# Optimization experiments

Hardware: AMD Instinct MI355X
Metric: run time of the kernel (lower is better)

Reference implementation:

```python
import jax, jax.numpy as jnp
import numpy as np

N, FIN, H, FOUT = 4096, 128, 4, 64
NEG_INF = -1e9


def _xavier(key, shape):
    fan_in, fan_out = shape[-2], shape[-1]
    limit = float(np.sqrt(6.0 / (fan_in + fan_out)))
    return jax.random.uniform(key, shape, jnp.float32, -limit, limit)


def setup_inputs() -> dict:
    key = jax.random.key(0)
    ks = jax.random.split(key, 7)
    x = jax.random.normal(ks[0], (N, FIN), jnp.float32)
    u = jax.random.uniform(ks[1], (N, N))
    mask = jnp.where(u < 0.02, 0.0, NEG_INF).astype(jnp.float32)
    idx = jnp.arange(N)
    mask = mask.at[idx, idx].set(0.0)
    proj_param = _xavier(ks[2], (H, FIN, FOUT))          # per-head projection
    score_src = _xavier(ks[3], (H, FOUT, 1))             # scoring_fn_source (IMP1 layout)
    score_tgt = _xavier(ks[4], (H, FOUT, 1))             # scoring_fn_target
    skip_w = _xavier(ks[5], (H * FOUT, FIN))             # skip_proj Linear weight
    bias = jnp.zeros((H * FOUT,), jnp.float32)
    return {"x": x, "mask": mask, "proj_param": proj_param,
            "score_src": score_src, "score_tgt": score_tgt,
            "skip_w": skip_w, "bias": bias}


def reference(x, mask, proj_param, score_src, score_tgt, skip_w, bias):
    # project: [1,N,Fin] @ [H,Fin,Fout] -> [H,N,Fout]
    h = jnp.einsum('nf,hfo->hno', x, proj_param)
    # additive (Bahdanau-style) scores
    s_src = jnp.matmul(h, score_src)                     # [H,N,1]
    s_tgt = jnp.matmul(h, score_tgt)                     # [H,N,1]
    all_scores = jax.nn.leaky_relu(s_src + jnp.swapaxes(s_tgt, 1, 2), 0.2)  # [H,N,N]
    attn = jax.nn.softmax(all_scores + mask[None, :, :], axis=-1)           # [H,N,N]
    # aggregate: [H,N,N] @ [H,N,Fout] -> [N,H,Fout]
    out = jnp.einsum('hnm,hmo->nho', attn, h)
    # skip connection (dims differ: Fin != H*Fout -> use skip_proj)
    out = out + jnp.matmul(x, skip_w.T).reshape(N, H, FOUT)
    out = out.reshape(N, H * FOUT) + bias                # concat heads + bias
    return jax.nn.elu(out)
```

## Files before the change

kernel.cpp:

```cpp
#include <hip/hip_runtime.h>
#include <hip/hip_bf16.h>
#include <math.h>


#define NN   4096
#define FIN  128
#define NH   4
#define FO   64
#define HF   256
#define MAXNBR 384

__global__ __launch_bounds__(256) void k1_gemm(
        const float* __restrict__ x,
        const float* __restrict__ proj,
        const float* __restrict__ skw,
        float* __restrict__ h_ws, float* __restrict__ skip_ws) {
    __shared__ float sA[64 * 132];
    __shared__ float sB[128 * 64];
    const int tid = threadIdx.x;
    const int bc  = blockIdx.x;
    const int i0  = blockIdx.y * 64;

    {
        const float4* src = (const float4*)(x + (size_t)i0 * FIN);
        #pragma unroll
        for (int q = 0; q < 8; q++) {
            int s   = tid + q * 256;
            int row = s >> 5;
            int c4  = (s & 31) << 2;
            float4 v = src[s];
            float* d = sA + row * 132 + c4;
            d[0] = v.x; d[1] = v.y; d[2] = v.z; d[3] = v.w;
        }
    }
    if (bc < 4) {
        const float4* src = (const float4*)(proj + (size_t)bc * FIN * FO);
        #pragma unroll
        for (int q = 0; q < 8; q++) {
            int s = tid + q * 256;
            *(float4*)(sB + (size_t)s * 4) = src[s];
        }
    } else {
        const float* sw = skw + (size_t)(bc - 4) * 64 * FIN;
        #pragma unroll
        for (int q = 0; q < 8; q++) {
            int s  = tid + q * 256;
            int c  = s & 63;
            int k4 = (s >> 6) << 2;
            float4 v = *(const float4*)(sw + (size_t)c * FIN + k4);
            sB[(k4 + 0) * 64 + c] = v.x;
            sB[(k4 + 1) * 64 + c] = v.y;
            sB[(k4 + 2) * 64 + c] = v.z;
            sB[(k4 + 3) * 64 + c] = v.w;
        }
    }
    __syncthreads();

    const int tx = tid & 15, ty = tid >> 4;
    const int r0 = ty << 2, c0 = tx << 2;
    float acc[4][4] = {};
    #pragma unroll 2
    for (int k = 0; k < FIN; k += 4) {
        alignas(16) float a[4][4];
        alignas(16) float b[4][4];
        #pragma unroll
        for (int rr = 0; rr < 4; rr++)
            *(float4*)a[rr] = *(const float4*)(sA + (r0 + rr) * 132 + k);
        #pragma unroll
        for (int kk = 0; kk < 4; kk++)
            *(float4*)b[kk] = *(const float4*)(sB + (k + kk) * 64 + c0);
        #pragma unroll
        for (int kk = 0; kk < 4; kk++)
            #pragma unroll
            for (int rr = 0; rr < 4; rr++)
                #pragma unroll
                for (int cc = 0; cc < 4; cc++)
                    acc[rr][cc] = fmaf(a[rr][kk], b[kk][cc], acc[rr][cc]);
    }

    if (bc < 4) {
        float* dst = h_ws + (size_t)bc * (NN * FO) + (size_t)i0 * FO;
        #pragma unroll
        for (int rr = 0; rr < 4; rr++)
            *(float4*)(dst + (size_t)(r0 + rr) * FO + c0) = *(float4*)acc[rr];
    } else {
        float* dst = skip_ws + (size_t)i0 * HF + (bc - 4) * 64;
        #pragma unroll
        for (int rr = 0; rr < 4; rr++)
            *(float4*)(dst + (size_t)(r0 + rr) * HF + c0) = *(float4*)acc[rr];
    }
}

__global__ __launch_bounds__(256) void k1b_scores(
        const float* __restrict__ h_ws,
        const float* __restrict__ asrc, const float* __restrict__ atgt,
        float* __restrict__ src4, float* __restrict__ tgt4) {
    const int lane = threadIdx.x & 63;
    const int w    = threadIdx.x >> 6;
    const int i    = blockIdx.x * 4 + w;
    float ss[4], tt[4];
    #pragma unroll
    for (int hh = 0; hh < 4; hh++) {
        float hv = h_ws[(size_t)hh * (NN * FO) + (size_t)i * FO + lane];
        float sv = hv * asrc[hh * FO + lane];
        float tv = hv * atgt[hh * FO + lane];
        #pragma unroll
        for (int off = 32; off >= 1; off >>= 1) {
            sv += __shfl_xor(sv, off, 64);
            tv += __shfl_xor(tv, off, 64);
        }
        ss[hh] = sv; tt[hh] = tv;
    }
    if (lane == 0) {
        *(float4*)(src4 + (size_t)i * 4) = make_float4(ss[0], ss[1], ss[2], ss[3]);
        *(float4*)(tgt4 + (size_t)i * 4) = make_float4(tt[0], tt[1], tt[2], tt[3]);
    }
}

__global__ __launch_bounds__(256) void k2_attn(
        const unsigned int* __restrict__ mask,
        const float* __restrict__ h_ws,
        const float* __restrict__ skip_ws,
        const float* __restrict__ src4,
        const float* __restrict__ tgt4,
        const float* __restrict__ bias,
        float* __restrict__ out) {
    __shared__ int   s_nbr[MAXNBR];
    __shared__ float s_p[4][MAXNBR];
    __shared__ int   s_cnt;
    __shared__ float s_red[4][4];
    __shared__ float s_m[4];
    __shared__ float s_l[4];
    const int tid = threadIdx.x;
    const int i   = blockIdx.x;
    if (tid == 0) s_cnt = 0;
    __syncthreads();

    const float4 sv4 = *(const float4*)(src4 + (size_t)i * 4);
    const float sc0 = sv4.x, sc1 = sv4.y, sc2 = sv4.z, sc3 = sv4.w;
    float mx0 = -1e30f, mx1 = -1e30f, mx2 = -1e30f, mx3 = -1e30f;

    const uint4* mrow = (const uint4*)(mask + (size_t)i * NN);
    #pragma unroll
    for (int q = 0; q < 4; q++) {
        int s = tid + q * 256;
        uint4 mv = mrow[s];
        int jb = s * 4;
        unsigned int wv[4] = {mv.x, mv.y, mv.z, mv.w};
        #pragma unroll
        for (int e = 0; e < 4; e++) {
            if ((wv[e] & 0x7fffffffu) == 0u) {
                int j = jb + e;
                int k = atomicAdd(&s_cnt, 1);
                if (k < MAXNBR) {
                    s_nbr[k] = j;
                    float4 tg = *(const float4*)(tgt4 + (size_t)j * 4);
                    float p0 = sc0 + tg.x; p0 = p0 > 0.f ? p0 : 0.2f * p0; s_p[0][k] = p0; mx0 = fmaxf(mx0, p0);
                    float p1 = sc1 + tg.y; p1 = p1 > 0.f ? p1 : 0.2f * p1; s_p[1][k] = p1; mx1 = fmaxf(mx1, p1);
                    float p2 = sc2 + tg.z; p2 = p2 > 0.f ? p2 : 0.2f * p2; s_p[2][k] = p2; mx2 = fmaxf(mx2, p2);
                    float p3 = sc3 + tg.w; p3 = p3 > 0.f ? p3 : 0.2f * p3; s_p[3][k] = p3; mx3 = fmaxf(mx3, p3);
                }
            }
        }
    }

    const int lane = tid & 63, wid = tid >> 6;
    {
        float mxa[4] = {mx0, mx1, mx2, mx3};
        #pragma unroll
        for (int h = 0; h < 4; h++) {
            float m = mxa[h];
            #pragma unroll
            for (int off = 32; off >= 1; off >>= 1) m = fmaxf(m, __shfl_xor(m, off, 64));
            if (lane == 0) s_red[wid][h] = m;
        }
    }
    __syncthreads();
    if (tid < 4)
        s_m[tid] = fmaxf(fmaxf(s_red[0][tid], s_red[1][tid]),
                         fmaxf(s_red[2][tid], s_red[3][tid]));
    __syncthreads();

    const int cnt = min(s_cnt, MAXNBR);
    const float m0 = s_m[0], m1 = s_m[1], m2 = s_m[2], m3 = s_m[3];
    float l0 = 0.f, l1 = 0.f, l2 = 0.f, l3 = 0.f;
    for (int k = tid; k < cnt; k += 256) {
        float p0 = __expf(s_p[0][k] - m0); s_p[0][k] = p0; l0 += p0;
        float p1 = __expf(s_p[1][k] - m1); s_p[1][k] = p1; l1 += p1;
        float p2 = __expf(s_p[2][k] - m2); s_p[2][k] = p2; l2 += p2;
        float p3 = __expf(s_p[3][k] - m3); s_p[3][k] = p3; l3 += p3;
    }
    {
        float la[4] = {l0, l1, l2, l3};
        #pragma unroll
        for (int h = 0; h < 4; h++) {
            float l = la[h];
            #pragma unroll
            for (int off = 32; off >= 1; off >>= 1) l += __shfl_xor(l, off, 64);
            if (lane == 0) s_red[wid][h] = l;
        }
    }
    __syncthreads();
    if (tid < 4)
        s_l[tid] = s_red[0][tid] + s_red[1][tid] + s_red[2][tid] + s_red[3][tid];
    __syncthreads();

    const int hh = tid >> 6;
    const int f  = tid & 63;
    const float* hp = h_ws + (size_t)hh * (NN * FO) + f;
    const float* pp = s_p[hh];
    const float lv  = s_l[hh];
    const float inv = (cnt > 0 && lv > 0.f) ? 1.0f / lv : 0.0f;
    float acc = 0.f;
    for (int k = 0; k < cnt; k++)
        acc = fmaf(pp[k], hp[(size_t)s_nbr[k] * FO], acc);

    float v = acc * inv + skip_ws[(size_t)i * HF + tid] + bias[tid];
    v = v > 0.f ? v : expm1f(v);
    out[(size_t)i * HF + tid] = v;
}

extern "C" void kernel_launch(void* const* d_in, const int* in_sizes, int n_in,
                              void* d_out, int out_size, void* d_ws, size_t ws_size,
                              hipStream_t stream) {
    const float*        x    = (const float*)d_in[0];
    const unsigned int* mask = (const unsigned int*)d_in[1];
    const float*        proj = (const float*)d_in[2];
    const float*        asrc = (const float*)d_in[3];
    const float*        atgt = (const float*)d_in[4];
    const float*        skw  = (const float*)d_in[5];
    const float*        bias = (const float*)d_in[6];
    float*              out  = (float*)d_out;

    float* ws      = (float*)d_ws;
    float* h_ws    = ws;
    float* skip_ws = ws + 1048576;
    float* src4    = ws + 2097152;
    float* tgt4    = ws + 2097152 + 16384;

    hipLaunchKernelGGL(k1_gemm, dim3(8, 64), dim3(256), 0, stream,
                       x, proj, skw, h_ws, skip_ws);
    hipLaunchKernelGGL(k1b_scores, dim3(1024), dim3(256), 0, stream,
                       h_ws, asrc, atgt, src4, tgt4);
    hipLaunchKernelGGL(k2_attn, dim3(4096), dim3(256), 0, stream,
                       mask, h_ws, skip_ws, src4, tgt4, bias, out);
}
```

Measured before the change: 155.9 us.

## Fuse score computation into GEMM, compact mask via ballot-free prefix scan, interleave heads

Computes the per-head source and target attention scores inside the projection GEMM epilogue with a shuffle reduction, removing the separate scores kernel. It also stores h in node-major [N, H*F] layout so each neighbor gather reads one contiguous 1 KB row across all heads. Mask compaction uses per-thread bitmasks and a wave prefix scan instead of shared-memory atomics, which also gives a deterministic neighbor order. The aggregation loop is unrolled by 8 to keep more gathers in flight. The cost is extra shuffles in the GEMM epilogue and another synchronisation stage in the attention kernel.

```diff
diff --git a/kernel.cpp b/kernel.cpp
--- a/kernel.cpp
+++ b/kernel.cpp
@@ -14,7 +14,10 @@
         const float* __restrict__ x,
         const float* __restrict__ proj,
         const float* __restrict__ skw,
-        float* __restrict__ h_ws, float* __restrict__ skip_ws) {
+        const float* __restrict__ asrc,
+        const float* __restrict__ atgt,
+        float* __restrict__ h2, float* __restrict__ skip_ws,
+        float* __restrict__ src4, float* __restrict__ tgt4) {
     __shared__ float sA[64 * 132];
     __shared__ float sB[128 * 64];
     const int tid = threadIdx.x;
@@ -79,10 +82,34 @@
     }
 
     if (bc < 4) {
-        float* dst = h_ws + (size_t)bc * (NN * FO) + (size_t)i0 * FO;
+        float* dst = h2 + (size_t)i0 * HF + bc * 64;
         #pragma unroll
         for (int rr = 0; rr < 4; rr++)
-            *(float4*)(dst + (size_t)(r0 + rr) * FO + c0) = *(float4*)acc[rr];
+            *(float4*)(dst + (size_t)(r0 + rr) * HF + c0) = *(float4*)acc[rr];
+
+        float as[4], at[4];
+        #pragma unroll
+        for (int cc = 0; cc < 4; cc++) {
+            as[cc] = asrc[bc * FO + c0 + cc];
+            at[cc] = atgt[bc * FO + c0 + cc];
+        }
+        #pragma unroll
+        for (int rr = 0; rr < 4; rr++) {
+            float ps = acc[rr][0] * as[0] + acc[rr][1] * as[1]
+                     + acc[rr][2] * as[2] + acc[rr][3] * as[3];
+            float pt = acc[rr][0] * at[0] + acc[rr][1] * at[1]
+                     + acc[rr][2] * at[2] + acc[rr][3] * at[3];
+            #pragma unroll
+            for (int off = 8; off >= 1; off >>= 1) {
+                ps += __shfl_xor(ps, off, 64);
+                pt += __shfl_xor(pt, off, 64);
+            }
+            if (tx == 0) {
+                int i = i0 + r0 + rr;
+                src4[(size_t)i * 4 + bc] = ps;
+                tgt4[(size_t)i * 4 + bc] = pt;
+            }
+        }
     } else {
         float* dst = skip_ws + (size_t)i0 * HF + (bc - 4) * 64;
         #pragma unroll
@@ -91,35 +118,9 @@
     }
 }
 
-__global__ __launch_bounds__(256) void k1b_scores(
-        const float* __restrict__ h_ws,
-        const float* __restrict__ asrc, const float* __restrict__ atgt,
-        float* __restrict__ src4, float* __restrict__ tgt4) {
-    const int lane = threadIdx.x & 63;
-    const int w    = threadIdx.x >> 6;
-    const int i    = blockIdx.x * 4 + w;
-    float ss[4], tt[4];
-    #pragma unroll
-    for (int hh = 0; hh < 4; hh++) {
-        float hv = h_ws[(size_t)hh * (NN * FO) + (size_t)i * FO + lane];
-        float sv = hv * asrc[hh * FO + lane];
-        float tv = hv * atgt[hh * FO + lane];
-        #pragma unroll
-        for (int off = 32; off >= 1; off >>= 1) {
-            sv += __shfl_xor(sv, off, 64);
-            tv += __shfl_xor(tv, off, 64);
-        }
-        ss[hh] = sv; tt[hh] = tv;
-    }
-    if (lane == 0) {
-        *(float4*)(src4 + (size_t)i * 4) = make_float4(ss[0], ss[1], ss[2], ss[3]);
-        *(float4*)(tgt4 + (size_t)i * 4) = make_float4(tt[0], tt[1], tt[2], tt[3]);
-    }
-}
-
 __global__ __launch_bounds__(256) void k2_attn(
         const unsigned int* __restrict__ mask,
-        const float* __restrict__ h_ws,
+        const float* __restrict__ h2,
         const float* __restrict__ skip_ws,
         const float* __restrict__ src4,
         const float* __restrict__ tgt4,
@@ -127,44 +128,59 @@
         float* __restrict__ out) {
     __shared__ int   s_nbr[MAXNBR];
     __shared__ float s_p[4][MAXNBR];
-    __shared__ int   s_cnt;
+    __shared__ int   s_wt[4];
     __shared__ float s_red[4][4];
     __shared__ float s_m[4];
     __shared__ float s_l[4];
-    const int tid = threadIdx.x;
-    const int i   = blockIdx.x;
-    if (tid == 0) s_cnt = 0;
+    const int tid  = threadIdx.x;
+    const int lane = tid & 63, wid = tid >> 6;
+    const int i    = blockIdx.x;
+
+    const uint4* mrow = (const uint4*)(mask + (size_t)i * NN);
+    uint4 mv0 = mrow[tid];
+    uint4 mv1 = mrow[tid + 256];
+    uint4 mv2 = mrow[tid + 512];
+    uint4 mv3 = mrow[tid + 768];
+    unsigned int hm = 0;
+#define TESTW(w, b) hm |= (((w) & 0x7fffffffu) == 0u ? (1u << (b)) : 0u)
+    TESTW(mv0.x, 0);  TESTW(mv0.y, 1);  TESTW(mv0.z, 2);  TESTW(mv0.w, 3);
+    TESTW(mv1.x, 4);  TESTW(mv1.y, 5);  TESTW(mv1.z, 6);  TESTW(mv1.w, 7);
+    TESTW(mv2.x, 8);  TESTW(mv2.y, 9);  TESTW(mv2.z, 10); TESTW(mv2.w, 11);
+    TESTW(mv3.x, 12); TESTW(mv3.y, 13); TESTW(mv3.z, 14); TESTW(mv3.w, 15);
+#undef TESTW
+    int nh = __popc(hm);
+    int v = nh;
+    #pragma unroll
+    for (int off = 1; off < 64; off <<= 1) {
+        int t = __shfl_up(v, off, 64);
+        if (lane >= off) v += t;
+    }
+    int excl = v - nh;
+    if (lane == 63) s_wt[wid] = v;
+    __syncthreads();
+    const int t0 = s_wt[0], t1 = s_wt[1], t2 = s_wt[2], t3 = s_wt[3];
+    const int cnt = min(t0 + t1 + t2 + t3, MAXNBR);
+    int k = (wid > 0 ? t0 : 0) + (wid > 1 ? t1 : 0) + (wid > 2 ? t2 : 0) + excl;
+    while (hm) {
+        int b = __ffs(hm) - 1;
+        hm &= hm - 1;
+        int j = ((tid + ((b >> 2) << 8)) << 2) + (b & 3);
+        if (k < MAXNBR) s_nbr[k] = j;
+        k++;
+    }
     __syncthreads();
 
     const float4 sv4 = *(const float4*)(src4 + (size_t)i * 4);
     const float sc0 = sv4.x, sc1 = sv4.y, sc2 = sv4.z, sc3 = sv4.w;
     float mx0 = -1e30f, mx1 = -1e30f, mx2 = -1e30f, mx3 = -1e30f;
-
-    const uint4* mrow = (const uint4*)(mask + (size_t)i * NN);
-    #pragma unroll
-    for (int q = 0; q < 4; q++) {
-        int s = tid + q * 256;
-        uint4 mv = mrow[s];
-        int jb = s * 4;
-        unsigned int wv[4] = {mv.x, mv.y, mv.z, mv.w};
-        #pragma unroll
-        for (int e = 0; e < 4; e++) {
-            if ((wv[e] & 0x7fffffffu) == 0u) {
-                int j = jb + e;
-                int k = atomicAdd(&s_cnt, 1);
-                if (k < MAXNBR) {
-                    s_nbr[k] = j;
-                    float4 tg = *(const float4*)(tgt4 + (size_t)j * 4);
-                    float p0 = sc0 + tg.x; p0 = p0 > 0.f ? p0 : 0.2f * p0; s_p[0][k] = p0; mx0 = fmaxf(mx0, p0);
-                    float p1 = sc1 + tg.y; p1 = p1 > 0.f ? p1 : 0.2f * p1; s_p[1][k] = p1; mx1 = fmaxf(mx1, p1);
-                    float p2 = sc2 + tg.z; p2 = p2 > 0.f ? p2 : 0.2f * p2; s_p[2][k] = p2; mx2 = fmaxf(mx2, p2);
-                    float p3 = sc3 + tg.w; p3 = p3 > 0.f ? p3 : 0.2f * p3; s_p[3][k] = p3; mx3 = fmaxf(mx3, p3);
-                }
-            }
-        }
-    }
-
-    const int lane = tid & 63, wid = tid >> 6;
+    for (int kk = tid; kk < cnt; kk += 256) {
+        int j = s_nbr[kk];
+        float4 tg = *(const float4*)(tgt4 + (size_t)j * 4);
+        float p0 = sc0 + tg.x; p0 = p0 > 0.f ? p0 : 0.2f * p0; s_p[0][kk] = p0; mx0 = fmaxf(mx0, p0);
+        float p1 = sc1 + tg.y; p1 = p1 > 0.f ? p1 : 0.2f * p1; s_p[1][kk] = p1; mx1 = fmaxf(mx1, p1);
+        float p2 = sc2 + tg.z; p2 = p2 > 0.f ? p2 : 0.2f * p2; s_p[2][kk] = p2; mx2 = fmaxf(mx2, p2);
+        float p3 = sc3 + tg.w; p3 = p3 > 0.f ? p3 : 0.2f * p3; s_p[3][kk] = p3; mx3 = fmaxf(mx3, p3);
+    }
     {
         float mxa[4] = {mx0, mx1, mx2, mx3};
         #pragma unroll
@@ -181,14 +197,13 @@
                          fmaxf(s_red[2][tid], s_red[3][tid]));
     __syncthreads();
 
-    const int cnt = min(s_cnt, MAXNBR);
     const float m0 = s_m[0], m1 = s_m[1], m2 = s_m[2], m3 = s_m[3];
     float l0 = 0.f, l1 = 0.f, l2 = 0.f, l3 = 0.f;
-    for (int k = tid; k < cnt; k += 256) {
-        float p0 = __expf(s_p[0][k] - m0); s_p[0][k] = p0; l0 += p0;
-        float p1 = __expf(s_p[1][k] - m1); s_p[1][k] = p1; l1 += p1;
-        float p2 = __expf(s_p[2][k] - m2); s_p[2][k] = p2; l2 += p2;
-        float p3 = __expf(s_p[3][k] - m3); s_p[3][k] = p3; l3 += p3;
+    for (int kk = tid; kk < cnt; kk += 256) {
+        float p0 = __expf(s_p[0][kk] - m0); s_p[0][kk] = p0; l0 += p0;
+        float p1 = __expf(s_p[1][kk] - m1); s_p[1][kk] = p1; l1 += p1;
+        float p2 = __expf(s_p[2][kk] - m2); s_p[2][kk] = p2; l2 += p2;
+        float p3 = __expf(s_p[3][kk] - m3); s_p[3][kk] = p3; l3 += p3;
     }
     {
         float la[4] = {l0, l1, l2, l3};
@@ -205,19 +220,35 @@
         s_l[tid] = s_red[0][tid] + s_red[1][tid] + s_red[2][tid] + s_red[3][tid];
     __syncthreads();
 
-    const int hh = tid >> 6;
-    const int f  = tid & 63;
-    const float* hp = h_ws + (size_t)hh * (NN * FO) + f;
-    const float* pp = s_p[hh];
-    const float lv  = s_l[hh];
+    const float* pp = s_p[wid];
+    const float lv  = s_l[wid];
     const float inv = (cnt > 0 && lv > 0.f) ? 1.0f / lv : 0.0f;
     float acc = 0.f;
-    for (int k = 0; k < cnt; k++)
-        acc = fmaf(pp[k], hp[(size_t)s_nbr[k] * FO], acc);
-
-    float v = acc * inv + skip_ws[(size_t)i * HF + tid] + bias[tid];
-    v = v > 0.f ? v : expm1f(v);
-    out[(size_t)i * HF + tid] = v;
+    int kk = 0;
+    for (; kk + 8 <= cnt; kk += 8) {
+        int   j0 = s_nbr[kk + 0], j1 = s_nbr[kk + 1], j2 = s_nbr[kk + 2], j3 = s_nbr[kk + 3];
+        int   j4 = s_nbr[kk + 4], j5 = s_nbr[kk + 5], j6 = s_nbr[kk + 6], j7 = s_nbr[kk + 7];
+        float p0 = pp[kk + 0], p1 = pp[kk + 1], p2 = pp[kk + 2], p3 = pp[kk + 3];
+        float p4 = pp[kk + 4], p5 = pp[kk + 5], p6 = pp[kk + 6], p7 = pp[kk + 7];
+        float h0 = h2[(size_t)j0 * HF + tid];
+        float h1 = h2[(size_t)j1 * HF + tid];
+        float h2v = h2[(size_t)j2 * HF + tid];
+        float h3 = h2[(size_t)j3 * HF + tid];
+        float h4 = h2[(size_t)j4 * HF + tid];
+        float h5 = h2[(size_t)j5 * HF + tid];
+        float h6 = h2[(size_t)j6 * HF + tid];
+        float h7 = h2[(size_t)j7 * HF + tid];
+        acc = fmaf(p0, h0, acc); acc = fmaf(p1, h1, acc);
+        acc = fmaf(p2, h2v, acc); acc = fmaf(p3, h3, acc);
+        acc = fmaf(p4, h4, acc); acc = fmaf(p5, h5, acc);
+        acc = fmaf(p6, h6, acc); acc = fmaf(p7, h7, acc);
+    }
+    for (; kk < cnt; kk++)
+        acc = fmaf(pp[kk], h2[(size_t)s_nbr[kk] * HF + tid], acc);
+
+    float vv = acc * inv + skip_ws[(size_t)i * HF + tid] + bias[tid];
+    vv = vv > 0.f ? vv : expm1f(vv);
+    out[(size_t)i * HF + tid] = vv;
 }
 
 extern "C" void kernel_launch(void* const* d_in, const int* in_sizes, int n_in,
@@ -233,15 +264,13 @@
     float*              out  = (float*)d_out;
 
     float* ws      = (float*)d_ws;
-    float* h_ws    = ws;
+    float* h2      = ws;
     float* skip_ws = ws + 1048576;
     float* src4    = ws + 2097152;
     float* tgt4    = ws + 2097152 + 16384;
 
     hipLaunchKernelGGL(k1_gemm, dim3(8, 64), dim3(256), 0, stream,
-                       x, proj, skw, h_ws, skip_ws);
-    hipLaunchKernelGGL(k1b_scores, dim3(1024), dim3(256), 0, stream,
-                       h_ws, asrc, atgt, src4, tgt4);
+                       x, proj, skw, asrc, atgt, h2, skip_ws, src4, tgt4);
     hipLaunchKernelGGL(k2_attn, dim3(4096), dim3(256), 0, stream,
-                       mask, h_ws, skip_ws, src4, tgt4, bias, out);
+                       mask, h2, skip_ws, src4, tgt4, bias, out);
 }
```

Result: faster. 137.0 us (-12.1%).
